# Performance work log

Hardware: AMD Instinct MI355X
Metric: run time of the kernel (lower is better)

## Reference

```python
import jax, jax.numpy as jnp
import numpy as np

N_EMBD = 1024
N_HEAD = 16
HEAD_DIM = N_EMBD // N_HEAD
B, T = 2, 2048
EPS = 1e-5


def _layernorm(x, gamma, beta):
    mu = jnp.mean(x, axis=-1, keepdims=True)
    var = jnp.mean((x - mu) ** 2, axis=-1, keepdims=True)
    return gamma * (x - mu) / jnp.sqrt(var + EPS) + beta


def setup_inputs() -> dict:
    key = jax.random.key(0)
    ks = jax.random.split(key, 12)
    s = 0.02
    d, f = N_EMBD, 4 * N_EMBD
    return {
        "x": jax.random.normal(ks[0], (B, T, d), dtype=jnp.float32),
        "ln1_g": jnp.ones((d,), jnp.float32),
        "ln1_b": jnp.zeros((d,), jnp.float32),
        "wq": jax.random.normal(ks[1], (d, d), jnp.float32) * s,
        "bq": jnp.zeros((d,), jnp.float32),
        "wk": jax.random.normal(ks[2], (d, d), jnp.float32) * s,
        "bk": jnp.zeros((d,), jnp.float32),
        "wv": jax.random.normal(ks[3], (d, d), jnp.float32) * s,
        "bv": jnp.zeros((d,), jnp.float32),
        "wo": jax.random.normal(ks[4], (d, d), jnp.float32) * s,
        "bo": jnp.zeros((d,), jnp.float32),
        "ln2_g": jnp.ones((d,), jnp.float32),
        "ln2_b": jnp.zeros((d,), jnp.float32),
        "w1": jax.random.normal(ks[5], (d, f), jnp.float32) * s,
        "b1": jnp.zeros((f,), jnp.float32),
        "w2": jax.random.normal(ks[6], (f, d), jnp.float32) * s,
        "b2": jnp.zeros((d,), jnp.float32),
    }


def reference(x, ln1_g, ln1_b, wq, bq, wk, bk, wv, bv, wo, bo,
              ln2_g, ln2_b, w1, b1, w2, b2):
    Bn, Tn, C = x.shape
    # --- attention branch (dropout = identity, eval mode) ---
    xn = _layernorm(x, ln1_g, ln1_b)
    q = (xn @ wq + bq).reshape(Bn, Tn, N_HEAD, HEAD_DIM)
    k = (xn @ wk + bk).reshape(Bn, Tn, N_HEAD, HEAD_DIM)
    v = (xn @ wv + bv).reshape(Bn, Tn, N_HEAD, HEAD_DIM)
    scale = 1.0 / jnp.sqrt(jnp.float32(HEAD_DIM))
    scores = jnp.einsum("bqhd,bkhd->bhqk", q, k) * scale  # [B,H,T,T]
    causal = jnp.tril(jnp.ones((Tn, Tn), dtype=bool))
    scores = jnp.where(causal[None, None], scores, -jnp.inf)
    weights = jax.nn.softmax(scores, axis=-1)
    attn = jnp.einsum("bhqk,bkhd->bqhd", weights, v).reshape(Bn, Tn, C)
    x = x + (attn @ wo + bo)
    # --- MLP branch ---
    h = _layernorm(x, ln2_g, ln2_b)
    h = jax.nn.gelu(h @ w1 + b1, approximate=False)
    x = x + (h @ w2 + b2)
    return x
```

## Files before the change

### kernel.cpp

```cpp
#include <hip/hip_runtime.h>
#include <stdint.h>

#define T_SEQ 2048
#define NHEAD 16
#define HDIM 64
#define CDIM 1024
#define FDIM 4096
#define MROWS 4096
#define NQB 32

typedef __bf16 bf16;
typedef __bf16 bf16x8 __attribute__((ext_vector_type(8)));
typedef float f32x4 __attribute__((ext_vector_type(4)));

__device__ __forceinline__ void gload_lds16(const void* g, void* l) {
  __builtin_amdgcn_global_load_lds(
      (const __attribute__((address_space(1))) void*)g,
      (__attribute__((address_space(3))) void*)l, 16, 0, 0);
}

__device__ __forceinline__ void wt_body(const float* __restrict__ src,
                                        bf16* __restrict__ dst, int K, int N,
                                        int k0, int n0) {
  __shared__ float tile[64][65];
  int tid = threadIdx.x;
  int r4 = tid >> 4, c4 = (tid & 15) * 4;
#pragma unroll
  for (int p = 0; p < 4; ++p) {
    int r = p * 16 + r4;
    float4 v = *(const float4*)&src[(size_t)(k0 + r) * N + n0 + c4];
    tile[r][c4] = v.x; tile[r][c4 + 1] = v.y;
    tile[r][c4 + 2] = v.z; tile[r][c4 + 3] = v.w;
  }
  __syncthreads();
  int n8 = tid >> 3, k8 = (tid & 7) * 8;
#pragma unroll
  for (int p = 0; p < 2; ++p) {
    int n = p * 32 + n8;
    union { bf16 h[8]; uint4 u; } t;
#pragma unroll
    for (int j = 0; j < 8; ++j) t.h[j] = (bf16)tile[k8 + j][n];
    *(uint4*)&dst[(size_t)(n0 + n) * K + k0 + k8] = t.u;
  }
}

__global__ void wt_kernel(const float* __restrict__ src, bf16* __restrict__ dst,
                          int K, int N) {
  wt_body(src, dst, K, N, blockIdx.y * 64, blockIdx.x * 64);
}

__global__ void wt4_kernel(const float* s0, const float* s1, const float* s2,
                           const float* s3, bf16* d0, bf16* d1, bf16* d2, bf16* d3) {
  const float* src = blockIdx.z == 0 ? s0 : blockIdx.z == 1 ? s1 : blockIdx.z == 2 ? s2 : s3;
  bf16* dst = blockIdx.z == 0 ? d0 : blockIdx.z == 1 ? d1 : blockIdx.z == 2 ? d2 : d3;
  wt_body(src, dst, 1024, 1024, blockIdx.y * 64, blockIdx.x * 64);
}

__global__ void vt_kernel(const bf16* __restrict__ v, bf16* __restrict__ vt) {
  __shared__ bf16 tile[64][65];
  int bh = blockIdx.y;
  int t0 = blockIdx.x * 64;
  int tid = threadIdx.x;
  const bf16* src = v + (size_t)bh * T_SEQ * HDIM;
  bf16* dst = vt + (size_t)bh * HDIM * T_SEQ;
  int r8 = tid >> 3, c8 = (tid & 7) * 8;
#pragma unroll
  for (int p = 0; p < 2; ++p) {
    int r = p * 32 + r8;
    union { uint4 u; bf16 h[8]; } t;
    t.u = *(const uint4*)&src[(size_t)(t0 + r) * HDIM + c8];
#pragma unroll
    for (int j = 0; j < 8; ++j) tile[r][c8 + j] = t.h[j];
  }
  __syncthreads();
#pragma unroll
  for (int p = 0; p < 2; ++p) {
    int d = p * 32 + r8;
    union { uint4 u; bf16 h[8]; } t;
#pragma unroll
    for (int j = 0; j < 8; ++j) t.h[j] = tile[c8 + j][d];
    *(uint4*)&dst[(size_t)d * T_SEQ + t0 + c8] = t.u;
  }
}

__global__ __launch_bounds__(256)
void ln_kernel(const float* __restrict__ x, const float* __restrict__ g,
               const float* __restrict__ b, bf16* __restrict__ out) {
  int row = blockIdx.x;
  int tid = threadIdx.x;
  float4 v = *(const float4*)&x[(size_t)row * CDIM + tid * 4];
  float s = v.x + v.y + v.z + v.w;
  float ss = v.x * v.x + v.y * v.y + v.z * v.z + v.w * v.w;
#pragma unroll
  for (int off = 1; off < 64; off <<= 1) {
    s += __shfl_xor(s, off, 64);
    ss += __shfl_xor(ss, off, 64);
  }
  __shared__ float red[8];
  int wv = tid >> 6, ln = tid & 63;
  if (ln == 0) { red[wv] = s; red[4 + wv] = ss; }
  __syncthreads();
  s = red[0] + red[1] + red[2] + red[3];
  ss = red[4] + red[5] + red[6] + red[7];
  float mu = s * (1.0f / CDIM);
  float var = ss * (1.0f / CDIM) - mu * mu;
  float rstd = rsqrtf(var + 1e-5f);
  float4 gv = *(const float4*)&g[tid * 4];
  float4 bv = *(const float4*)&b[tid * 4];
  union { bf16 h[4]; uint2 u; } o;
  o.h[0] = (bf16)(gv.x * (v.x - mu) * rstd + bv.x);
  o.h[1] = (bf16)(gv.y * (v.y - mu) * rstd + bv.y);
  o.h[2] = (bf16)(gv.z * (v.z - mu) * rstd + bv.z);
  o.h[3] = (bf16)(gv.w * (v.w - mu) * rstd + bv.w);
  *(uint2*)&out[(size_t)row * CDIM + tid * 4] = o.u;
}

enum { EPI_QKV = 0, EPI_F32RES = 1, EPI_GELU = 2 };

template <int EPI>
__global__ __launch_bounds__(512, 1)
void gemm256(const bf16* __restrict__ A, const bf16* __restrict__ Bt,
             const float* __restrict__ bias, const float* __restrict__ bias2,
             const float* __restrict__ bias3, const float* res,
             void* outp, void* out2, void* out3, int M, int N, int K) {
  __shared__ __align__(16) bf16 As[3][256 * 32];
  __shared__ __align__(16) bf16 Bs[3][256 * 32];
  int tid = threadIdx.x;
  int w = tid >> 6, l = tid & 63;
  int wr = w >> 2, wc = w & 3;
  int lo = l & 15, g = l >> 4;

  int nwg = gridDim.x * gridDim.y;
  int orig = blockIdx.y * gridDim.x + blockIdx.x;
  int lid = (orig & 7) * (nwg >> 3) + (orig >> 3);
  int bx = lid % gridDim.x, by = lid / gridDim.x;
  int m0 = by * 256, n0 = bx * 256;

  f32x4 acc[8][4];
#pragma unroll
  for (int i = 0; i < 8; ++i)
#pragma unroll
    for (int j = 0; j < 4; ++j) acc[i][j] = (f32x4){0.f, 0.f, 0.f, 0.f};

  const bf16* Ab = A + (size_t)m0 * K;
  const bf16* Bb = Bt + (size_t)n0 * K;

  int srow = tid >> 2;
  int scol = ((tid & 3) ^ ((tid >> 3) & 3)) * 8;
  auto STAGE_A = [&](int t, int buf) {
    int k0 = t * 32;
#pragma unroll
    for (int c = 0; c < 2; ++c)
      gload_lds16(Ab + (size_t)(c * 128 + srow) * K + k0 + scol,
                  &As[buf][c * 4096 + w * 512]);
  };
  auto STAGE_B = [&](int t, int buf) {
    int k0 = t * 32;
#pragma unroll
    for (int c = 0; c < 2; ++c)
      gload_lds16(Bb + (size_t)(c * 128 + srow) * K + k0 + scol,
                  &Bs[buf][c * 4096 + w * 512]);
  };

  int nt = K >> 5;
  STAGE_A(0, 0); STAGE_B(0, 0);
  STAGE_A(1, 1); STAGE_B(1, 1);
  asm volatile("s_waitcnt vmcnt(4)" ::: "memory");
  __syncthreads();
  int sw = (lo >> 1) & 3;
  int b0 = 0;
  for (int t = 0; t < nt; ++t) {
    int b2 = b0 - 1; if (b2 < 0) b2 += 3;
    bf16x8 af[4], bfr[4];
#pragma unroll
    for (int m = 0; m < 4; ++m) {
      int R = wr * 128 + m * 16 + lo;
      af[m] = *(const bf16x8*)&As[b0][R * 32 + (g ^ sw) * 8];
    }
#pragma unroll
    for (int n = 0; n < 4; ++n) {
      int R = wc * 64 + n * 16 + lo;
      bfr[n] = *(const bf16x8*)&Bs[b0][R * 32 + (g ^ sw) * 8];
    }
    if (t + 2 < nt) STAGE_A(t + 2, b2);
    asm volatile("s_barrier" ::: "memory");
    __builtin_amdgcn_s_setprio(1);
#pragma unroll
    for (int m = 0; m < 4; ++m)
#pragma unroll
      for (int n = 0; n < 4; ++n)
        acc[m][n] = __builtin_amdgcn_mfma_f32_16x16x32_bf16(af[m], bfr[n], acc[m][n], 0, 0, 0);
    __builtin_amdgcn_s_setprio(0);
#pragma unroll
    for (int m = 0; m < 4; ++m) {
      int R = wr * 128 + (m + 4) * 16 + lo;
      af[m] = *(const bf16x8*)&As[b0][R * 32 + (g ^ sw) * 8];
    }
    if (t + 2 < nt) {
      STAGE_B(t + 2, b2);
      asm volatile("s_waitcnt vmcnt(4)" ::: "memory");
    } else if (t + 1 < nt) {
      asm volatile("s_waitcnt vmcnt(0)" ::: "memory");
    }
    asm volatile("s_barrier" ::: "memory");
    __builtin_amdgcn_s_setprio(1);
#pragma unroll
    for (int m = 0; m < 4; ++m)
#pragma unroll
      for (int n = 0; n < 4; ++n)
        acc[m + 4][n] = __builtin_amdgcn_mfma_f32_16x16x32_bf16(af[m], bfr[n], acc[m + 4][n], 0, 0, 0);
    __builtin_amdgcn_s_setprio(0);
    b0 = (b0 == 2) ? 0 : b0 + 1;
  }

  if constexpr (EPI == EPI_QKV) {
    int which = n0 >> 10;
    const float* bb = which == 0 ? bias : (which == 1 ? bias2 : bias3);
    bf16* ob = (bf16*)(which == 0 ? outp : (which == 1 ? out2 : out3));
#pragma unroll
    for (int m = 0; m < 8; ++m)
#pragma unroll
      for (int n = 0; n < 4; ++n)
#pragma unroll
        for (int j = 0; j < 4; ++j) {
          int row = m0 + wr * 128 + m * 16 + g * 4 + j;
          int col = n0 + wc * 64 + n * 16 + lo;
          int cw = col & (CDIM - 1);
          float v = acc[m][n][j] + bb[cw];
          int b = row >> 11, tt = row & (T_SEQ - 1);
          int h = cw >> 6, d = cw & (HDIM - 1);
          ob[(((size_t)(b * NHEAD + h)) * T_SEQ + tt) * HDIM + d] = (bf16)v;
        }
  } else {
#pragma unroll
    for (int m = 0; m < 8; ++m)
#pragma unroll
      for (int n = 0; n < 4; ++n)
#pragma unroll
        for (int j = 0; j < 4; ++j) {
          int row = m0 + wr * 128 + m * 16 + g * 4 + j;
          int col = n0 + wc * 64 + n * 16 + lo;
          float v = acc[m][n][j] + bias[col];
          if constexpr (EPI == EPI_F32RES) {
            ((float*)outp)[(size_t)row * N + col] = v + res[(size_t)row * N + col];
          } else {
            float ge = 0.5f * v * (1.0f + erff(v * 0.70710678118654752f));
            ((bf16*)outp)[(size_t)row * N + col] = (bf16)ge;
          }
        }
  }
}

template <int EPI, int TN>
__global__ __launch_bounds__(256, 2)
void gemm_bt(const bf16* __restrict__ A, const bf16* __restrict__ Bt,
             const float* __restrict__ bias, const float* __restrict__ bias2,
             const float* __restrict__ bias3, const float* res,
             void* outp, void* out2, void* out3, int M, int N, int K) {
  constexpr int MR = (TN == 128) ? 4 : 2;
  __shared__ __align__(16) bf16 As[4][128 * 32];
  __shared__ __align__(16) bf16 Bs[4][TN * 32];
  int tid = threadIdx.x;
  int w = tid >> 6, l = tid & 63;
  int lo = l & 15, g = l >> 4;
  int rowb = (TN == 128) ? (w >> 1) * 64 : w * 32;
  int colb = (TN == 128) ? (w & 1) * 64 : 0;

  int nwg = gridDim.x * gridDim.y;
  int orig = blockIdx.y * gridDim.x + blockIdx.x;
  int lid = (orig & 7) * (nwg >> 3) + (orig >> 3);
  int bx = lid % gridDim.x, by = lid / gridDim.x;
  int m0 = by * 128, n0 = bx * TN;

  f32x4 acc[MR][4];
#pragma unroll
  for (int i = 0; i < MR; ++i)
#pragma unroll
    for (int j = 0; j < 4; ++j) acc[i][j] = (f32x4){0.f, 0.f, 0.f, 0.f};

  const bf16* Ab = A + (size_t)m0 * K;
  const bf16* Bb = Bt + (size_t)n0 * K;

  auto STAGE = [&](int t, int buf) {
    int k0 = t * 32;
    int row = (l >> 2);
    int col = ((l & 3) ^ ((l >> 3) & 3)) * 8;
#pragma unroll
    for (int i = 0; i < 2; ++i) {
      int c = w * 2 + i;
      gload_lds16(Ab + (size_t)(c * 16 + row) * K + k0 + col, &As[buf][c * 512]);
    }
    if constexpr (TN == 128) {
#pragma unroll
      for (int i = 0; i < 2; ++i) {
        int c = w * 2 + i;
        gload_lds16(Bb + (size_t)(c * 16 + row) * K + k0 + col, &Bs[buf][c * 512]);
      }
    } else {
      int c = w;
      gload_lds16(Bb + (size_t)(c * 16 + row) * K + k0 + col, &Bs[buf][c * 512]);
    }
  };

  int nt = K >> 5;
  STAGE(0, 0);
  STAGE(1, 1);
  STAGE(2, 2);
  int sw = (lo >> 1) & 3;
  for (int t = 0; t < nt; ++t) {
    if constexpr (TN == 128) {
      if (t + 2 < nt)      asm volatile("s_waitcnt vmcnt(8)" ::: "memory");
      else if (t + 1 < nt) asm volatile("s_waitcnt vmcnt(4)" ::: "memory");
      else                 asm volatile("s_waitcnt vmcnt(0)" ::: "memory");
    } else {
      if (t + 2 < nt)      asm volatile("s_waitcnt vmcnt(6)" ::: "memory");
      else if (t + 1 < nt) asm volatile("s_waitcnt vmcnt(3)" ::: "memory");
      else                 asm volatile("s_waitcnt vmcnt(0)" ::: "memory");
    }
    __builtin_amdgcn_s_barrier();
    __builtin_amdgcn_sched_barrier(0);
    int cur = t & 3;
    bf16x8 af[MR], bfr[4];
#pragma unroll
    for (int m = 0; m < MR; ++m) {
      int R = rowb + m * 16 + lo;
      af[m] = *(const bf16x8*)&As[cur][R * 32 + (g ^ sw) * 8];
    }
#pragma unroll
    for (int n = 0; n < 4; ++n) {
      int R = colb + n * 16 + lo;
      bfr[n] = *(const bf16x8*)&Bs[cur][R * 32 + (g ^ sw) * 8];
    }
    if (t + 3 < nt) STAGE(t + 3, (t + 3) & 3);
    __builtin_amdgcn_s_setprio(1);
#pragma unroll
    for (int m = 0; m < MR; ++m)
#pragma unroll
      for (int n = 0; n < 4; ++n)
        acc[m][n] = __builtin_amdgcn_mfma_f32_16x16x32_bf16(af[m], bfr[n], acc[m][n], 0, 0, 0);
    __builtin_amdgcn_s_setprio(0);
  }

#pragma unroll
  for (int m = 0; m < MR; ++m)
#pragma unroll
    for (int n = 0; n < 4; ++n)
#pragma unroll
      for (int j = 0; j < 4; ++j) {
        int row = m0 + rowb + m * 16 + g * 4 + j;
        int col = n0 + colb + n * 16 + lo;
        float v = acc[m][n][j] + bias[col];
        if constexpr (EPI == EPI_F32RES) {
          ((float*)outp)[(size_t)row * N + col] = v + res[(size_t)row * N + col];
        } else {
          float ge = 0.5f * v * (1.0f + erff(v * 0.70710678118654752f));
          ((bf16*)outp)[(size_t)row * N + col] = (bf16)ge;
        }
      }
}

__device__ __forceinline__ void attn_tile(
    const bf16* __restrict__ Ksb, const bf16* __restrict__ Vsb,
    bf16* __restrict__ Psw, const bf16x8 qf[2], f32x4 Ot[4],
    float& mrun, float& lrun, int lo, int g, int kbase, int myq, bool diag) {
  f32x4 st[4];
#pragma unroll
  for (int kt = 0; kt < 4; ++kt) {
    f32x4 a = (f32x4){0.f, 0.f, 0.f, 0.f};
#pragma unroll
    for (int dh = 0; dh < 2; ++dh) {
      int R = kt * 16 + lo;
      int slot = (dh * 4 + g) ^ (R & 7);
      bf16x8 kf = *(const bf16x8*)&Ksb[R * 64 + slot * 8];
      a = __builtin_amdgcn_mfma_f32_16x16x32_bf16(kf, qf[dh], a, 0, 0, 0);
    }
    st[kt] = a;
  }
  if (diag) {
#pragma unroll
    for (int kt = 0; kt < 4; ++kt)
#pragma unroll
      for (int j = 0; j < 4; ++j) {
        int key = kbase + kt * 16 + g * 4 + j;
        if (key > myq) st[kt][j] = -1e30f;
      }
  }
  float cmax = -1e30f;
#pragma unroll
  for (int kt = 0; kt < 4; ++kt)
#pragma unroll
    for (int j = 0; j < 4; ++j) cmax = fmaxf(cmax, st[kt][j]);
  cmax = fmaxf(cmax, __shfl_xor(cmax, 16, 64));
  cmax = fmaxf(cmax, __shfl_xor(cmax, 32, 64));
  float mnew = fmaxf(mrun, cmax);
  float corr = exp2f(mrun - mnew);
  float csum = 0.f;
#pragma unroll
  for (int kt = 0; kt < 4; ++kt) {
    union { bf16 h[4]; uint2 u; } pk;
#pragma unroll
    for (int j = 0; j < 4; ++j) {
      float pv = exp2f(st[kt][j] - mnew);
      csum += pv;
      pk.h[j] = (bf16)pv;
    }
    *(uint2*)&Psw[lo * 72 + kt * 16 + g * 4] = pk.u;
  }
  csum += __shfl_xor(csum, 16, 64);
  csum += __shfl_xor(csum, 32, 64);
  lrun = lrun * corr + csum;
  mrun = mnew;
#pragma unroll
  for (int dt = 0; dt < 4; ++dt)
#pragma unroll
    for (int j = 0; j < 4; ++j) Ot[dt][j] *= corr;
#pragma unroll
  for (int ks = 0; ks < 2; ++ks) {
    bf16x8 pf = *(const bf16x8*)&Psw[lo * 72 + ks * 32 + g * 8];
#pragma unroll
    for (int dt = 0; dt < 4; ++dt) {
      int R = dt * 16 + lo;
      int slot = (ks * 4 + g) ^ (R & 7);
      bf16x8 vf = *(const bf16x8*)&Vsb[R * 64 + slot * 8];
      Ot[dt] = __builtin_amdgcn_mfma_f32_16x16x32_bf16(vf, pf, Ot[dt], 0, 0, 0);
    }
  }
}

__global__ __launch_bounds__(256, 2)
void attn_kernel(const bf16* __restrict__ q, const bf16* __restrict__ k,
                 const bf16* __restrict__ vt, bf16* __restrict__ out) {
  __shared__ __align__(16) bf16 Ks[2][64 * 64];
  __shared__ __align__(16) bf16 Vs[2][64 * 64];
  __shared__ __align__(16) bf16 Ps[4][16 * 72];
  int tid = threadIdx.x;
  int w = tid >> 6, l = tid & 63;
  int lo = l & 15, g = l >> 4;
  int nwg = gridDim.x * gridDim.y;
  int orig = blockIdx.y * gridDim.x + blockIdx.x;
  int lid = (orig & 7) * (nwg >> 3) + (orig >> 3);
  int p = lid & 15;
  int bh = lid >> 4;
  int qA = p, qB = NQB - 1 - p;
  int nch = qB + 1;
  const bf16* qh = q + (size_t)bh * T_SEQ * HDIM;
  const bf16* kh = k + (size_t)bh * T_SEQ * HDIM;
  const bf16* vh = vt + (size_t)bh * HDIM * T_SEQ;

  const float sc = 0.125f * 1.44269504f;
  bf16x8 qfA[2], qfB[2];
#pragma unroll
  for (int dh = 0; dh < 2; ++dh) {
    bf16x8 tA = *(const bf16x8*)&qh[(size_t)(qA * 64 + w * 16 + lo) * HDIM + dh * 32 + g * 8];
    bf16x8 tB = *(const bf16x8*)&qh[(size_t)(qB * 64 + w * 16 + lo) * HDIM + dh * 32 + g * 8];
#pragma unroll
    for (int j = 0; j < 8; ++j) {
      qfA[dh][j] = (bf16)((float)tA[j] * sc);
      qfB[dh][j] = (bf16)((float)tB[j] * sc);
    }
  }
  int myqA = qA * 64 + w * 16 + lo;
  int myqB = qB * 64 + w * 16 + lo;

  f32x4 OtA[4], OtB[4];
#pragma unroll
  for (int i = 0; i < 4; ++i) {
    OtA[i] = (f32x4){0.f, 0.f, 0.f, 0.f};
    OtB[i] = (f32x4){0.f, 0.f, 0.f, 0.f};
  }
  float mA = -1e30f, lA = 0.f, mB = -1e30f, lB = 0.f;

  int srow8 = l >> 3, s0 = l & 7;
  auto STAGE = [&](int kc, int buf) {
#pragma unroll
    for (int i = 0; i < 2; ++i) {
      int c = w * 2 + i;
      int r = c * 8 + srow8;
      int ecol = (s0 ^ (r & 7)) * 8;
      gload_lds16(&kh[(size_t)(kc * 64 + r) * HDIM + ecol], &Ks[buf][c * 512]);
      gload_lds16(&vh[(size_t)r * T_SEQ + kc * 64 + ecol], &Vs[buf][c * 512]);
    }
  };

  STAGE(0, 0);
  int cur = 0;
  for (int kc = 0; kc < nch; ++kc) {
    __syncthreads();
    if (kc + 1 < nch) STAGE(kc + 1, cur ^ 1);
    attn_tile(Ks[cur], Vs[cur], Ps[w], qfB, OtB, mB, lB, lo, g, kc * 64, myqB,
              kc == nch - 1);
    if (kc <= p)
      attn_tile(Ks[cur], Vs[cur], Ps[w], qfA, OtA, mA, lA, lo, g, kc * 64, myqA,
                kc == p);
    cur ^= 1;
  }

  int b = bh >> 4, h = bh & 15;
  {
    float inv = 1.0f / lA;
    bf16* ob = out + (((size_t)b * T_SEQ + myqA) * NHEAD + h) * HDIM;
#pragma unroll
    for (int dt = 0; dt < 4; ++dt)
#pragma unroll
      for (int j = 0; j < 4; ++j) ob[dt * 16 + g * 4 + j] = (bf16)(OtA[dt][j] * inv);
  }
  {
    float inv = 1.0f / lB;
    bf16* ob = out + (((size_t)b * T_SEQ + myqB) * NHEAD + h) * HDIM;
#pragma unroll
    for (int dt = 0; dt < 4; ++dt)
#pragma unroll
      for (int j = 0; j < 4; ++j) ob[dt * 16 + g * 4 + j] = (bf16)(OtB[dt][j] * inv);
  }
}

extern "C" void kernel_launch(void* const* d_in, const int* in_sizes, int n_in,
                              void* d_out, int out_size, void* d_ws, size_t ws_size,
                              hipStream_t stream) {
  (void)in_sizes; (void)n_in; (void)out_size; (void)ws_size;
  const float* x     = (const float*)d_in[0];
  const float* ln1_g = (const float*)d_in[1];
  const float* ln1_b = (const float*)d_in[2];
  const float* wq    = (const float*)d_in[3];
  const float* bq    = (const float*)d_in[4];
  const float* wk    = (const float*)d_in[5];
  const float* bk    = (const float*)d_in[6];
  const float* wv    = (const float*)d_in[7];
  const float* bv    = (const float*)d_in[8];
  const float* wo    = (const float*)d_in[9];
  const float* bo    = (const float*)d_in[10];
  const float* ln2_g = (const float*)d_in[11];
  const float* ln2_b = (const float*)d_in[12];
  const float* w1    = (const float*)d_in[13];
  const float* b1    = (const float*)d_in[14];
  const float* w2    = (const float*)d_in[15];
  const float* b2    = (const float*)d_in[16];
  float* out = (float*)d_out;

  const size_t MB = 1024ull * 1024ull;
  char* ws = (char*)d_ws;
  bf16* wqkvT = (bf16*)(ws + 0 * MB);
  bf16* wqT = wqkvT;
  bf16* wkT = (bf16*)(ws + 2 * MB);
  bf16* wvT = (bf16*)(ws + 4 * MB);
  bf16* woT = (bf16*)(ws + 6 * MB);
  bf16* w1T = (bf16*)(ws + 8 * MB);
  bf16* w2T = (bf16*)(ws + 16 * MB);
  bf16* xn  = (bf16*)(ws + 24 * MB);
  bf16* qb_ = (bf16*)(ws + 32 * MB);
  bf16* kb_ = (bf16*)(ws + 40 * MB);
  bf16* vb_ = (bf16*)(ws + 48 * MB);
  bf16* vtb = (bf16*)(ws + 56 * MB);
  bf16* aout = (bf16*)(ws + 24 * MB);
  bf16* hn  = (bf16*)(ws + 32 * MB);
  bf16* hb  = (bf16*)(ws + 40 * MB);

  dim3 blk(256);
  wt4_kernel<<<dim3(16, 16, 4), blk, 0, stream>>>(wq, wk, wv, wo, wqT, wkT, wvT, woT);
  wt_kernel<<<dim3(64, 16), blk, 0, stream>>>(w1, w1T, 1024, 4096);
  wt_kernel<<<dim3(16, 64), blk, 0, stream>>>(w2, w2T, 4096, 1024);

  ln_kernel<<<MROWS, blk, 0, stream>>>(x, ln1_g, ln1_b, xn);

  gemm256<EPI_QKV><<<dim3(12, 16), dim3(512), 0, stream>>>(
      xn, wqkvT, bq, bk, bv, nullptr, qb_, kb_, vb_, MROWS, 3 * CDIM, CDIM);

  vt_kernel<<<dim3(32, 32), blk, 0, stream>>>(vb_, vtb);
  attn_kernel<<<dim3(16, 32), blk, 0, stream>>>(qb_, kb_, vtb, aout);

  gemm_bt<EPI_F32RES, 64><<<dim3(16, 32), blk, 0, stream>>>(
      aout, woT, bo, nullptr, nullptr, x, out, nullptr, nullptr, MROWS, CDIM, CDIM);

  ln_kernel<<<MROWS, blk, 0, stream>>>(out, ln2_g, ln2_b, hn);

  gemm256<EPI_GELU><<<dim3(16, 16), dim3(512), 0, stream>>>(
      hn, w1T, b1, nullptr, nullptr, nullptr, hb, nullptr, nullptr, MROWS, FDIM, CDIM);
  gemm_bt<EPI_F32RES, 64><<<dim3(16, 32), blk, 0, stream>>>(
      hb, w2T, b2, nullptr, nullptr, out, out, nullptr, nullptr, MROWS, CDIM, FDIM);
}
```

Baseline: 241.4 us.

## Split-K the MLP down-projection GEMM and reduce partials with an add kernel

The final w2 GEMM (K=4096) now runs as a two-way split-K with 128-wide N tiles instead of 64-wide tiles and no split. The first K-half writes bias plus residual into the output and the second half writes raw partial sums to a scratch buffer. A separate vectorized kernel then adds the partial buffer into the output. The aim is to shorten the long K loop per block and get better tile reuse, at the cost of an extra 16 MB write and read of float partials and one more launch.

```diff
diff --git a/kernel.cpp b/kernel.cpp
--- a/kernel.cpp
+++ b/kernel.cpp
@@ -115,7 +115,19 @@
   *(uint2*)&out[(size_t)row * CDIM + tid * 4] = o.u;
 }
 
-enum { EPI_QKV = 0, EPI_F32RES = 1, EPI_GELU = 2 };
+__global__ __launch_bounds__(256)
+void addp_kernel(float* __restrict__ out, const float* __restrict__ p1, int n4) {
+  int i = blockIdx.x * 256 + threadIdx.x;
+  int stride = gridDim.x * 256;
+  for (; i < n4; i += stride) {
+    f32x4 a = *(const f32x4*)&out[i * 4];
+    f32x4 b = *(const f32x4*)&p1[i * 4];
+    a += b;
+    *(f32x4*)&out[i * 4] = a;
+  }
+}
+
+enum { EPI_QKV = 0, EPI_F32RES = 1, EPI_GELU = 2, EPI_SPLIT = 3 };
 
 template <int EPI>
 __global__ __launch_bounds__(512, 1)
@@ -256,7 +268,7 @@
 void gemm_bt(const bf16* __restrict__ A, const bf16* __restrict__ Bt,
              const float* __restrict__ bias, const float* __restrict__ bias2,
              const float* __restrict__ bias3, const float* res,
-             void* outp, void* out2, void* out3, int M, int N, int K) {
+             void* outp, void* out2, void* out3, int M, int N, int K, int Kstride) {
   constexpr int MR = (TN == 128) ? 4 : 2;
   __shared__ __align__(16) bf16 As[4][128 * 32];
   __shared__ __align__(16) bf16 Bs[4][TN * 32];
@@ -271,6 +283,7 @@
   int lid = (orig & 7) * (nwg >> 3) + (orig >> 3);
   int bx = lid % gridDim.x, by = lid / gridDim.x;
   int m0 = by * 128, n0 = bx * TN;
+  int koff = blockIdx.z * K;
 
   f32x4 acc[MR][4];
 #pragma unroll
@@ -278,8 +291,8 @@
 #pragma unroll
     for (int j = 0; j < 4; ++j) acc[i][j] = (f32x4){0.f, 0.f, 0.f, 0.f};
 
-  const bf16* Ab = A + (size_t)m0 * K;
-  const bf16* Bb = Bt + (size_t)n0 * K;
+  const bf16* Ab = A + (size_t)m0 * Kstride + koff;
+  const bf16* Bb = Bt + (size_t)n0 * Kstride + koff;
 
   auto STAGE = [&](int t, int buf) {
     int k0 = t * 32;
@@ -288,17 +301,17 @@
 #pragma unroll
     for (int i = 0; i < 2; ++i) {
       int c = w * 2 + i;
-      gload_lds16(Ab + (size_t)(c * 16 + row) * K + k0 + col, &As[buf][c * 512]);
+      gload_lds16(Ab + (size_t)(c * 16 + row) * Kstride + k0 + col, &As[buf][c * 512]);
     }
     if constexpr (TN == 128) {
 #pragma unroll
       for (int i = 0; i < 2; ++i) {
         int c = w * 2 + i;
-        gload_lds16(Bb + (size_t)(c * 16 + row) * K + k0 + col, &Bs[buf][c * 512]);
+        gload_lds16(Bb + (size_t)(c * 16 + row) * Kstride + k0 + col, &Bs[buf][c * 512]);
       }
     } else {
       int c = w;
-      gload_lds16(Bb + (size_t)(c * 16 + row) * K + k0 + col, &Bs[buf][c * 512]);
+      gload_lds16(Bb + (size_t)(c * 16 + row) * Kstride + k0 + col, &Bs[buf][c * 512]);
     }
   };
 
@@ -349,12 +362,21 @@
       for (int j = 0; j < 4; ++j) {
         int row = m0 + rowb + m * 16 + g * 4 + j;
         int col = n0 + colb + n * 16 + lo;
-        float v = acc[m][n][j] + bias[col];
-        if constexpr (EPI == EPI_F32RES) {
-          ((float*)outp)[(size_t)row * N + col] = v + res[(size_t)row * N + col];
+        if constexpr (EPI == EPI_SPLIT) {
+          if (blockIdx.z == 0) {
+            float v = acc[m][n][j] + bias[col];
+            ((float*)outp)[(size_t)row * N + col] = v + res[(size_t)row * N + col];
+          } else {
+            ((float*)out2)[(size_t)row * N + col] = acc[m][n][j];
+          }
         } else {
-          float ge = 0.5f * v * (1.0f + erff(v * 0.70710678118654752f));
-          ((bf16*)outp)[(size_t)row * N + col] = (bf16)ge;
+          float v = acc[m][n][j] + bias[col];
+          if constexpr (EPI == EPI_F32RES) {
+            ((float*)outp)[(size_t)row * N + col] = v + res[(size_t)row * N + col];
+          } else {
+            float ge = 0.5f * v * (1.0f + erff(v * 0.70710678118654752f));
+            ((bf16*)outp)[(size_t)row * N + col] = (bf16)ge;
+          }
         }
       }
 }
@@ -554,6 +576,7 @@
   bf16* aout = (bf16*)(ws + 24 * MB);
   bf16* hn  = (bf16*)(ws + 32 * MB);
   bf16* hb  = (bf16*)(ws + 40 * MB);
+  float* p1 = (float*)(ws + 24 * MB);
 
   dim3 blk(256);
   wt4_kernel<<<dim3(16, 16, 4), blk, 0, stream>>>(wq, wk, wv, wo, wqT, wkT, wvT, woT);
@@ -569,12 +592,14 @@
   attn_kernel<<<dim3(16, 32), blk, 0, stream>>>(qb_, kb_, vtb, aout);
 
   gemm_bt<EPI_F32RES, 64><<<dim3(16, 32), blk, 0, stream>>>(
-      aout, woT, bo, nullptr, nullptr, x, out, nullptr, nullptr, MROWS, CDIM, CDIM);
+      aout, woT, bo, nullptr, nullptr, x, out, nullptr, nullptr, MROWS, CDIM, CDIM, CDIM);
 
   ln_kernel<<<MROWS, blk, 0, stream>>>(out, ln2_g, ln2_b, hn);
 
   gemm256<EPI_GELU><<<dim3(16, 16), dim3(512), 0, stream>>>(
       hn, w1T, b1, nullptr, nullptr, nullptr, hb, nullptr, nullptr, MROWS, FDIM, CDIM);
-  gemm_bt<EPI_F32RES, 64><<<dim3(16, 32), blk, 0, stream>>>(
-      hb, w2T, b2, nullptr, nullptr, out, out, nullptr, nullptr, MROWS, CDIM, FDIM);
-}
+
+  gemm_bt<EPI_SPLIT, 128><<<dim3(8, 32, 2), blk, 0, stream>>>(
+      hb, w2T, b2, nullptr, nullptr, out, out, p1, nullptr, MROWS, CDIM, FDIM / 2, FDIM);
+  addp_kernel<<<2048, blk, 0, stream>>>(out, p1, MROWS * CDIM / 4);
+}
```

After: 248.0 us. 1.03x slower.
